# Kernel optimization log

Hardware: AMD Instinct MI355X
Metric: run time of the kernel (lower is better)

## Reference

```python
import jax, jax.numpy as jnp
import numpy as np

B, L, D, H = 4, 2048, 256, 8
FF = 128  # ff_intermediary_depth hard-coded in module
EPS = 1e-5


def layer_norm(x, g, b):
    mu = jnp.mean(x, axis=-1, keepdims=True)
    var = jnp.mean(jnp.square(x - mu), axis=-1, keepdims=True)
    return (x - mu) * jax.lax.rsqrt(var + EPS) * g + b


def setup_inputs() -> dict:
    key = jax.random.key(0)
    ks = jax.random.split(key, 8)
    s = 1.0 / np.sqrt(D)
    return {
        "seq": jax.random.normal(ks[0], (B, L, D), dtype=jnp.float32),
        "Wq": jax.random.normal(ks[1], (D, D * H), dtype=jnp.float32) * s,
        "Wk": jax.random.normal(ks[2], (D, D * H), dtype=jnp.float32) * s,
        "Wv": jax.random.normal(ks[3], (D, D * H), dtype=jnp.float32) * s,
        "Wo": jax.random.normal(ks[4], (D * H, D), dtype=jnp.float32) * (1.0 / np.sqrt(D * H)),
        "ln1_g": jnp.ones((D,), jnp.float32),
        "ln1_b": jnp.zeros((D,), jnp.float32),
        "W1": jax.random.normal(ks[5], (D, FF), dtype=jnp.float32) * s,
        "b1": jnp.zeros((FF,), jnp.float32),
        "W2": jax.random.normal(ks[6], (FF, D), dtype=jnp.float32) * (1.0 / np.sqrt(FF)),
        "b2": jnp.zeros((D,), jnp.float32),
        "ln2_g": jnp.ones((D,), jnp.float32),
        "ln2_b": jnp.zeros((D,), jnp.float32),
    }


def reference(seq, Wq, Wk, Wv, Wo, ln1_g, ln1_b, W1, b1, W2, b2, ln2_g, ln2_b):
    b, l, d = seq.shape
    # per-head dim equals full depth d (module quirk)
    q = (seq @ Wq).reshape(b, l, H, d)
    k = (seq @ Wk).reshape(b, l, H, d)
    v = (seq @ Wv).reshape(b, l, H, d)
    scores = jnp.einsum('bqhd,bkhd->bhqk', q, k) / jnp.sqrt(jnp.float32(d))
    a = jax.nn.softmax(scores, axis=-1)
    heads = jnp.einsum('bhqk,bkhd->bqhd', a, v).reshape(b, l, H * d)
    att_out = heads @ Wo
    x = layer_norm(seq + att_out, ln1_g, ln1_b)
    ff = jax.nn.relu(x @ W1 + b1) @ W2 + b2
    return layer_norm(x + ff, ln2_g, ln2_b)
```

## Files before the change

kernel.cpp:

```cpp
#include <hip/hip_runtime.h>


typedef unsigned short u16;
typedef unsigned int   u32;
typedef __bf16 bf16x8 __attribute__((ext_vector_type(8)));
typedef float  f32x4  __attribute__((ext_vector_type(4)));

#define MFMA(a, b, c) __builtin_amdgcn_mfma_f32_16x16x32_bf16(a, b, c, 0, 0, 0)

__device__ __forceinline__ float b2f(u16 h) {
  return __uint_as_float(((u32)h) << 16);
}
__device__ __forceinline__ u16 f2b(float f) {
  u32 u = __float_as_uint(f);
  u += 0x7FFFu + ((u >> 16) & 1u);
  return (u16)(u >> 16);
}
__device__ __forceinline__ bf16x8 ldb8(const u16* p) { return *(const bf16x8*)p; }

typedef const __attribute__((address_space(1))) u32* gas1_t;
typedef __attribute__((address_space(3))) u32* las3_t;
__device__ __forceinline__ void gload_lds16(const u16* g, u16* lds_base) {
  __builtin_amdgcn_global_load_lds((gas1_t)(const void*)g,
                                   (las3_t)(void*)lds_base, 16, 0, 0);
}

__device__ __forceinline__ int detect_f32(const void* seq) {
  const u32* s = (const u32*)seq;
  int cnt = 0;
  #pragma unroll
  for (int i = 0; i < 64; i++) {
    u32 e = (s[i] >> 7) & 0xFFu;
    cnt += (e >= 100u && e <= 140u) ? 1 : 0;
  }
  return cnt < 48;
}

__device__ __forceinline__ u16 ldw(const void* W, size_t idx, int isf32) {
  return isf32 ? f2b(((const float*)W)[idx]) : ((const u16*)W)[idx];
}

__global__ __launch_bounds__(256) void ingest_kernel(
    const void* __restrict__ seq, const void* __restrict__ g1,
    const void* __restrict__ be1, const void* __restrict__ b1,
    const void* __restrict__ b2v, const void* __restrict__ g2,
    const void* __restrict__ be2, u16* __restrict__ sbuf,
    u16* __restrict__ vecs) {
  int isf32 = detect_f32(seq);
  int bx = blockIdx.x, tid = threadIdx.x;
  if (bx < 2048) {
    size_t i = (size_t)bx * 1024 + tid * 4;
    if (isf32) {
      const float* sp = (const float*)seq;
      u16 o0 = f2b(sp[i]), o1 = f2b(sp[i + 1]), o2 = f2b(sp[i + 2]), o3 = f2b(sp[i + 3]);
      uint2 ov; ov.x = (u32)o0 | ((u32)o1 << 16); ov.y = (u32)o2 | ((u32)o3 << 16);
      *(uint2*)(sbuf + i) = ov;
    } else {
      *(uint2*)(sbuf + i) = ((const uint2*)seq)[i >> 2];
    }
  } else {
    int t = bx - 2048;
    const void* src; int n;
    switch (t) {
      case 0: src = g1;  n = 256; break;
      case 1: src = be1; n = 256; break;
      case 2: src = b1;  n = 128; break;
      case 3: src = b2v; n = 256; break;
      case 4: src = g2;  n = 256; break;
      default: src = be2; n = 256; break;
    }
    if (tid < n) vecs[t * 256 + tid] = ldw(src, tid, isf32);
  }
}

__global__ __launch_bounds__(256) void pack_kernel(
    const void* __restrict__ Wq, const void* __restrict__ Wk,
    const void* __restrict__ Wv, const void* __restrict__ Wo,
    const void* __restrict__ W1, const void* __restrict__ W2,
    const void* __restrict__ seq,
    u16* __restrict__ pWq, u16* __restrict__ pWk, u16* __restrict__ pWv,
    u16* __restrict__ pWo, u16* __restrict__ pW1, u16* __restrict__ pW2) {
  int isf32 = detect_f32(seq);
  const void* W; u16* P; int K, N;
  switch (blockIdx.y) {
    case 0: W = Wq; P = pWq; K = 256;  N = 2048; break;
    case 1: W = Wk; P = pWk; K = 256;  N = 2048; break;
    case 2: W = Wv; P = pWv; K = 256;  N = 2048; break;
    case 3: W = Wo; P = pWo; K = 2048; N = 256;  break;
    case 4: W = W1; P = pW1; K = 256;  N = 128;  break;
    default: W = W2; P = pW2; K = 128; N = 256;  break;
  }
  int t = blockIdx.x * 256 + threadIdx.x;
  int total = (K >> 5) * (N >> 4) * 64;
  if (t >= total) return;
  int lane = t & 63, f = t >> 6;
  int NT = N >> 4;
  int kt = f / NT, nt = f - kt * NT;
  int row0 = kt * 32 + ((lane >> 4) << 3);
  int col = nt * 16 + (lane & 15);
  u16 e[8];
  #pragma unroll
  for (int j = 0; j < 8; j++) e[j] = ldw(W, (size_t)(row0 + j) * N + col, isf32);
  uint4 u;
  u.x = (u32)e[0] | ((u32)e[1] << 16);
  u.y = (u32)e[2] | ((u32)e[3] << 16);
  u.z = (u32)e[4] | ((u32)e[5] << 16);
  u.w = (u32)e[6] | ((u32)e[7] << 16);
  *(uint4*)(P + ((size_t)f * 64 + lane) * 8) = u;
}

__global__ __launch_bounds__(256) void qkv_kernel(
    const u16* __restrict__ X,
    const u16* __restrict__ pWq, const u16* __restrict__ pWk,
    const u16* __restrict__ pWv,
    u16* __restrict__ Qo, u16* __restrict__ Ko, u16* __restrict__ Vo,
    int ntbase, int hc) {
  __shared__ u16 blds[64 * 512];
  const u16* Pw = (blockIdx.z == 0) ? pWq : ((blockIdx.z == 1) ? pWk : pWv);
  u16* Out = (blockIdx.z == 0) ? Qo : ((blockIdx.z == 1) ? Ko : Vo);
  int tid = threadIdx.x, lane = tid & 63, w = tid >> 6;
  int nt0 = ntbase + blockIdx.x * 8;
  #pragma unroll
  for (int i = 0; i < 16; i++) {
    int u = tid + i * 256;
    int fl = u >> 6, q = u & 63;
    int kt = fl >> 3, nt = fl & 7;
    ((uint4*)blds)[u] = ((const uint4*)Pw)[(size_t)(kt * 128 + nt0 + nt) * 64 + q];
  }
  __syncthreads();
  int m0 = blockIdx.y * 128 + w * 32;
  f32x4 acc[2][8] = {};
  #pragma unroll
  for (int kt = 0; kt < 8; kt++) {
    bf16x8 a0 = ldb8(X + (size_t)(m0 + (lane & 15)) * 256 + kt * 32 + (lane >> 4) * 8);
    bf16x8 a1 = ldb8(X + (size_t)(m0 + 16 + (lane & 15)) * 256 + kt * 32 + (lane >> 4) * 8);
    const u16* bp = blds + (size_t)kt * 8 * 512 + (size_t)lane * 8;
    #pragma unroll
    for (int nt = 0; nt < 8; nt++) {
      bf16x8 b = ldb8(bp + nt * 512);
      acc[0][nt] = MFMA(a0, b, acc[0][nt]);
      acc[1][nt] = MFMA(a1, b, acc[1][nt]);
    }
  }
  int isv = (blockIdx.z == 2);
  int hl = blockIdx.x >> 1;
  int dd0 = (blockIdx.x & 1) * 128;
  int m0b = blockIdx.y * 128;
  int bi = m0b >> 11, l0 = m0b & 2047;
  __syncthreads();
  if (!isv) {
    #pragma unroll
    for (int mt = 0; mt < 2; mt++)
      #pragma unroll
      for (int nt = 0; nt < 8; nt++)
        #pragma unroll
        for (int r = 0; r < 4; r++)
          blds[(w * 32 + mt * 16 + (lane >> 4) * 4 + r) * 136 + nt * 16 + (lane & 15)] =
              f2b(acc[mt][nt][r]);
    __syncthreads();
    #pragma unroll
    for (int i = 0; i < 8; i++) {
      int c = tid + i * 256;
      int mloc = c >> 4, q = c & 15;
      uint4 v = *(uint4*)(blds + mloc * 136 + q * 8);
      *(uint4*)(Out + ((size_t)(bi * hc + hl) * 2048 + l0 + mloc) * 256 + dd0 + q * 8) = v;
    }
  } else {
    #pragma unroll
    for (int mt = 0; mt < 2; mt++)
      #pragma unroll
      for (int nt = 0; nt < 8; nt++)
        #pragma unroll
        for (int r = 0; r < 4; r++)
          blds[(nt * 16 + (lane & 15)) * 136 + w * 32 + mt * 16 + (lane >> 4) * 4 + r] =
              f2b(acc[mt][nt][r]);
    __syncthreads();
    #pragma unroll
    for (int i = 0; i < 8; i++) {
      int c = tid + i * 256;
      int nloc = c >> 4, q = c & 15;
      uint4 v = *(uint4*)(blds + nloc * 136 + q * 8);
      *(uint4*)(Out + ((size_t)(bi * hc + hl) * 256 + dd0 + nloc) * 2048 + l0 + q * 8) = v;
    }
  }
}

__global__ __launch_bounds__(256, 2) void attn_kernel(
    const u16* __restrict__ Q, const u16* __restrict__ K,
    const u16* __restrict__ Vt, u16* __restrict__ O, int nbh) {
  __shared__ u16 kbuf[2 * 8192];
  __shared__ u16 vbuf[2 * 8192];
  __shared__ u16 plds[4 * 1280];
  int tid = threadIdx.x, lane = tid & 63, w = tid >> 6;
  int bi2 = blockIdx.x;
  int bh, qt;
  if (nbh >= 8) {
    int G = nbh >> 3;
    bh = (bi2 & 7) * G + (bi2 >> 3) % G;
    qt = bi2 / (8 * G);
  } else {
    bh = bi2 % nbh; qt = bi2 / nbh;
  }
  const u16* Qb  = Q  + (size_t)bh * 2048 * 256;
  const u16* Kb  = K  + (size_t)bh * 2048 * 256;
  const u16* Vtb = Vt + (size_t)bh * 256 * 2048;
  u16* Ob = O + (size_t)bh * 2048 * 256;
  int q0 = qt * 128 + w * 32;
  bf16x8 qf[2][8];
  #pragma unroll
  for (int qq = 0; qq < 2; qq++)
    #pragma unroll
    for (int kt = 0; kt < 8; kt++)
      qf[qq][kt] = ldb8(Qb + (size_t)(q0 + qq * 16 + (lane & 15)) * 256 +
                        kt * 32 + (lane >> 4) * 8);
  f32x4 o[2][16] = {};
  float lsum[2] = {0.f, 0.f};
  const float cexp = 0.0625f * 1.44269504088896f;
  u16* pl = plds + (size_t)w * 1280;

  #pragma unroll
  for (int j = 0; j < 4; j++) {
    int f = w * 4 + j;
    gload_lds16(Kb + (size_t)((f >> 3) * 16 + (lane & 15)) * 256 +
                    (f & 7) * 32 + (lane >> 4) * 8,
                kbuf + f * 512);
    gload_lds16(Vtb + (size_t)(f * 16 + (lane & 15)) * 2048 + (lane >> 4) * 8,
                vbuf + f * 512);
  }

  for (int t = 0; t < 64; t++) {
    int s0 = t * 32;
    asm volatile("s_waitcnt vmcnt(0)\ns_barrier" ::: "memory");
    if (t < 63) {
      int nb = (t + 1) & 1;
      #pragma unroll
      for (int j = 0; j < 4; j++) {
        int f = w * 4 + j;
        gload_lds16(Kb + (size_t)(s0 + 32 + (f >> 3) * 16 + (lane & 15)) * 256 +
                        (f & 7) * 32 + (lane >> 4) * 8,
                    kbuf + nb * 8192 + f * 512);
        gload_lds16(Vtb + (size_t)(f * 16 + (lane & 15)) * 2048 + s0 + 32 +
                        (lane >> 4) * 8,
                    vbuf + nb * 8192 + f * 512);
      }
    }
    const u16* kb = kbuf + (t & 1) * 8192;
    f32x4 s[2][2] = {};
    __builtin_amdgcn_s_setprio(1);
    #pragma unroll
    for (int ntk = 0; ntk < 2; ntk++)
      #pragma unroll
      for (int kt = 0; kt < 8; kt++) {
        bf16x8 a = ldb8(kb + (size_t)(ntk * 8 + kt) * 512 + lane * 8);
        s[0][ntk] = MFMA(a, qf[0][kt], s[0][ntk]);
        s[1][ntk] = MFMA(a, qf[1][kt], s[1][ntk]);
      }
    __builtin_amdgcn_s_setprio(0);
    #pragma unroll
    for (int qq = 0; qq < 2; qq++)
      #pragma unroll
      for (int ntk = 0; ntk < 2; ntk++) {
        float p0 = exp2f(s[qq][ntk][0] * cexp);
        float p1 = exp2f(s[qq][ntk][1] * cexp);
        float p2 = exp2f(s[qq][ntk][2] * cexp);
        float p3 = exp2f(s[qq][ntk][3] * cexp);
        lsum[qq] += (p0 + p1) + (p2 + p3);
        uint2 pk;
        pk.x = (u32)f2b(p0) | ((u32)f2b(p1) << 16);
        pk.y = (u32)f2b(p2) | ((u32)f2b(p3) << 16);
        *(uint2*)(pl + (qq * 16 + (lane & 15)) * 40 + 16 * ntk + 4 * (lane >> 4)) = pk;
      }
    asm volatile("s_waitcnt lgkmcnt(0)" ::: "memory");
    bf16x8 pa0 = ldb8(pl + (lane & 15) * 40 + (lane >> 4) * 8);
    bf16x8 pa1 = ldb8(pl + (16 + (lane & 15)) * 40 + (lane >> 4) * 8);
    const u16* vb0 = vbuf + (t & 1) * 8192;
    __builtin_amdgcn_s_setprio(1);
    #pragma unroll
    for (int nt = 0; nt < 16; nt++) {
      bf16x8 vb = ldb8(vb0 + (size_t)nt * 512 + lane * 8);
      o[0][nt] = MFMA(vb, pa0, o[0][nt]);
      o[1][nt] = MFMA(vb, pa1, o[1][nt]);
    }
    __builtin_amdgcn_s_setprio(0);
  }
  u16* el = kbuf + w * 1152;
  __syncthreads();
  #pragma unroll
  for (int qq = 0; qq < 2; qq++) {
    float l = lsum[qq];
    l += __shfl_xor(l, 16);
    l += __shfl_xor(l, 32);
    float linv = 1.0f / l;
    #pragma unroll
    for (int g = 0; g < 4; g++) {
      if (qq || g) asm volatile("s_waitcnt lgkmcnt(0)" ::: "memory");
      #pragma unroll
      for (int t2 = 0; t2 < 4; t2++) {
        int nt = g * 4 + t2;
        uint2 pk;
        pk.x = (u32)f2b(o[qq][nt][0] * linv) | ((u32)f2b(o[qq][nt][1] * linv) << 16);
        pk.y = (u32)f2b(o[qq][nt][2] * linv) | ((u32)f2b(o[qq][nt][3] * linv) << 16);
        *(uint2*)(el + (lane & 15) * 72 + t2 * 16 + 4 * (lane >> 4)) = pk;
      }
      asm volatile("s_waitcnt lgkmcnt(0)" ::: "memory");
      #pragma unroll
      for (int rep = 0; rep < 2; rep++) {
        int ch = lane + rep * 64;
        int row = ch >> 3, c8 = ch & 7;
        uint4 v = *(uint4*)(el + row * 72 + c8 * 8);
        *(uint4*)(Ob + (size_t)(q0 + qq * 16 + row) * 256 + g * 64 + c8 * 8) = v;
      }
    }
  }
}

__global__ __launch_bounds__(256) void accum_ln1_kernel(
    const u16* __restrict__ Oc, const u16* __restrict__ pWo,
    const u16* __restrict__ sbuf, const u16* __restrict__ vecs,
    u16* __restrict__ xout) {
  __shared__ u16 blds[64 * 512];
  int tid = threadIdx.x, lane = tid & 63, w = tid >> 6;
  int m0 = blockIdx.x * 64 + w * 16;
  int arow = m0 + (lane & 15);
  int bq = arow >> 11, lrow = arow & 2047;
  f32x4 acc[16] = {};
  for (int k0 = 0; k0 < 64; k0 += 4) {
    __syncthreads();
    #pragma unroll
    for (int i = 0; i < 16; i++) {
      int u = tid + i * 256;
      int fl = u >> 6, q = u & 63;
      int ktg = k0 + (fl >> 4), nt = fl & 15;
      ((uint4*)blds)[u] = ((const uint4*)pWo)[(size_t)(ktg * 16 + nt) * 64 + q];
    }
    __syncthreads();
    #pragma unroll
    for (int kl = 0; kl < 4; kl++) {
      int ktl = k0 + kl;
      int hl = ktl >> 3;
      int d0 = (ktl & 7) * 32 + (lane >> 4) * 8;
      bf16x8 a = ldb8(Oc + ((size_t)(bq * 8 + hl) * 2048 + lrow) * 256 + d0);
      const u16* bp = blds + (size_t)kl * 16 * 512 + (size_t)lane * 8;
      #pragma unroll
      for (int nt = 0; nt < 16; nt++) {
        bf16x8 b = ldb8(bp + nt * 512);
        acc[nt] = MFMA(a, b, acc[nt]);
      }
    }
  }
  int rbase = m0 + (lane >> 4) * 4;
  #pragma unroll
  for (int nt = 0; nt < 16; nt++) {
    int d = nt * 16 + (lane & 15);
    #pragma unroll
    for (int r = 0; r < 4; r++)
      acc[nt][r] += b2f(sbuf[(size_t)(rbase + r) * 256 + d]);
  }
  float mu[4], rs[4];
  #pragma unroll
  for (int r = 0; r < 4; r++) {
    float sm = 0.f;
    #pragma unroll
    for (int nt = 0; nt < 16; nt++) sm += acc[nt][r];
    sm += __shfl_xor(sm, 1); sm += __shfl_xor(sm, 2);
    sm += __shfl_xor(sm, 4); sm += __shfl_xor(sm, 8);
    mu[r] = sm * (1.0f / 256.0f);
    float v = 0.f;
    #pragma unroll
    for (int nt = 0; nt < 16; nt++) { float dd = acc[nt][r] - mu[r]; v += dd * dd; }
    v += __shfl_xor(v, 1); v += __shfl_xor(v, 2);
    v += __shfl_xor(v, 4); v += __shfl_xor(v, 8);
    rs[r] = rsqrtf(v * (1.0f / 256.0f) + 1e-5f);
  }
  #pragma unroll
  for (int nt = 0; nt < 16; nt++) {
    int d = nt * 16 + (lane & 15);
    float gg = b2f(vecs[d]), bb = b2f(vecs[256 + d]);
    #pragma unroll
    for (int r = 0; r < 4; r++)
      xout[(size_t)(rbase + r) * 256 + d] = f2b((acc[nt][r] - mu[r]) * rs[r] * gg + bb);
  }
}

__global__ __launch_bounds__(256) void accum_kernel(
    const u16* __restrict__ Oc, const u16* __restrict__ pWo,
    float* __restrict__ att_out, int kt0, int hc) {
  __shared__ u16 blds[64 * 512];
  int tid = threadIdx.x, lane = tid & 63, w = tid >> 6;
  int m0 = blockIdx.x * 64 + w * 16;
  int arow = m0 + (lane & 15);
  int bq = arow >> 11, lrow = arow & 2047;
  int ktn = hc * 8;
  f32x4 acc[16] = {};
  for (int k0 = 0; k0 < ktn; k0 += 4) {
    __syncthreads();
    #pragma unroll
    for (int i = 0; i < 16; i++) {
      int u = tid + i * 256;
      int fl = u >> 6, q = u & 63;
      int ktg = kt0 + k0 + (fl >> 4), nt = fl & 15;
      ((uint4*)blds)[u] = ((const uint4*)pWo)[(size_t)(ktg * 16 + nt) * 64 + q];
    }
    __syncthreads();
    #pragma unroll
    for (int kl = 0; kl < 4; kl++) {
      int ktl = k0 + kl;
      int hl = ktl >> 3;
      int d0 = (ktl & 7) * 32 + (lane >> 4) * 8;
      bf16x8 a = ldb8(Oc + ((size_t)(bq * hc + hl) * 2048 + lrow) * 256 + d0);
      const u16* bp = blds + (size_t)kl * 16 * 512 + (size_t)lane * 8;
      #pragma unroll
      for (int nt = 0; nt < 16; nt++) {
        bf16x8 b = ldb8(bp + nt * 512);
        acc[nt] = MFMA(a, b, acc[nt]);
      }
    }
  }
  int rbase = m0 + (lane >> 4) * 4;
  #pragma unroll
  for (int nt = 0; nt < 16; nt++) {
    int d = nt * 16 + (lane & 15);
    #pragma unroll
    for (int r = 0; r < 4; r++)
      att_out[(size_t)(rbase + r) * 256 + d] += acc[nt][r];
  }
}

__global__ __launch_bounds__(256) void ln1_kernel(
    const float* __restrict__ att_out, const u16* __restrict__ sbuf,
    const u16* __restrict__ vecs, u16* __restrict__ xout) {
  int tid = threadIdx.x, lane = tid & 63, w = tid >> 6;
  int row = blockIdx.x * 4 + w;
  const float* ar = att_out + (size_t)row * 256;
  f32x4 a = *(const f32x4*)(ar + lane * 4);
  uint2 sv = *(const uint2*)(sbuf + (size_t)row * 256 + lane * 4);
  float y[4];
  y[0] = a[0] + b2f((u16)(sv.x & 0xFFFF));
  y[1] = a[1] + b2f((u16)(sv.x >> 16));
  y[2] = a[2] + b2f((u16)(sv.y & 0xFFFF));
  y[3] = a[3] + b2f((u16)(sv.y >> 16));
  float sm = y[0] + y[1] + y[2] + y[3];
  sm += __shfl_xor(sm, 1);  sm += __shfl_xor(sm, 2);  sm += __shfl_xor(sm, 4);
  sm += __shfl_xor(sm, 8);  sm += __shfl_xor(sm, 16); sm += __shfl_xor(sm, 32);
  float mu = sm * (1.0f / 256.0f);
  float v = 0.f;
  #pragma unroll
  for (int j = 0; j < 4; j++) { float d = y[j] - mu; v += d * d; }
  v += __shfl_xor(v, 1);  v += __shfl_xor(v, 2);  v += __shfl_xor(v, 4);
  v += __shfl_xor(v, 8);  v += __shfl_xor(v, 16); v += __shfl_xor(v, 32);
  float rs = rsqrtf(v * (1.0f / 256.0f) + 1e-5f);
  u16 o[4];
  #pragma unroll
  for (int j = 0; j < 4; j++) {
    int d = lane * 4 + j;
    o[j] = f2b((y[j] - mu) * rs * b2f(vecs[d]) + b2f(vecs[256 + d]));
  }
  uint2 ov; ov.x = (u32)o[0] | ((u32)o[1] << 16); ov.y = (u32)o[2] | ((u32)o[3] << 16);
  *(uint2*)(xout + (size_t)row * 256 + lane * 4) = ov;
}

__global__ __launch_bounds__(256) void ffn_ln2_kernel(
    const u16* __restrict__ x, const u16* __restrict__ pW1,
    const u16* __restrict__ pW2, const u16* __restrict__ vecs,
    const void* __restrict__ seq, void* __restrict__ out) {
  __shared__ u16 hbuf[4 * 16 * 136];
  int isf32 = detect_f32(seq);
  int tid = threadIdx.x, lane = tid & 63, w = tid >> 6;
  int m0 = blockIdx.x * 64 + w * 16;
  int arow = m0 + (lane & 15);
  u16* hb = hbuf + w * 16 * 136;
  f32x4 acc1[8] = {};
  #pragma unroll
  for (int kt = 0; kt < 8; kt++) {
    bf16x8 a = ldb8(x + (size_t)arow * 256 + kt * 32 + (lane >> 4) * 8);
    const u16* bp = pW1 + ((size_t)kt * 8 * 64 + lane) * 8;
    #pragma unroll
    for (int nt = 0; nt < 8; nt++) {
      bf16x8 b = ldb8(bp + nt * 512);
      acc1[nt] = MFMA(a, b, acc1[nt]);
    }
  }
  #pragma unroll
  for (int nt = 0; nt < 8; nt++) {
    int col = nt * 16 + (lane & 15);
    float bb = b2f(vecs[512 + col]);
    #pragma unroll
    for (int r = 0; r < 4; r++) {
      float h = fmaxf(acc1[nt][r] + bb, 0.f);
      hb[((lane >> 4) * 4 + r) * 136 + col] = f2b(h);
    }
  }
  __syncthreads();
  f32x4 acc2[16] = {};
  #pragma unroll
  for (int ks = 0; ks < 4; ks++) {
    bf16x8 a = ldb8(hb + (lane & 15) * 136 + ks * 32 + (lane >> 4) * 8);
    const u16* bp = pW2 + ((size_t)ks * 16 * 64 + lane) * 8;
    #pragma unroll
    for (int nt = 0; nt < 16; nt++) {
      bf16x8 b = ldb8(bp + nt * 512);
      acc2[nt] = MFMA(a, b, acc2[nt]);
    }
  }
  int rbase = m0 + (lane >> 4) * 4;
  #pragma unroll
  for (int nt = 0; nt < 16; nt++) {
    int d = nt * 16 + (lane & 15);
    float bb = b2f(vecs[768 + d]);
    #pragma unroll
    for (int r = 0; r < 4; r++)
      acc2[nt][r] += bb + b2f(x[(size_t)(rbase + r) * 256 + d]);
  }
  float mu[4], rs[4];
  #pragma unroll
  for (int r = 0; r < 4; r++) {
    float sm = 0.f;
    #pragma unroll
    for (int nt = 0; nt < 16; nt++) sm += acc2[nt][r];
    sm += __shfl_xor(sm, 1); sm += __shfl_xor(sm, 2);
    sm += __shfl_xor(sm, 4); sm += __shfl_xor(sm, 8);
    mu[r] = sm * (1.0f / 256.0f);
    float v = 0.f;
    #pragma unroll
    for (int nt = 0; nt < 16; nt++) { float dd = acc2[nt][r] - mu[r]; v += dd * dd; }
    v += __shfl_xor(v, 1); v += __shfl_xor(v, 2);
    v += __shfl_xor(v, 4); v += __shfl_xor(v, 8);
    rs[r] = rsqrtf(v * (1.0f / 256.0f) + 1e-5f);
  }
  #pragma unroll
  for (int nt = 0; nt < 16; nt++) {
    int d = nt * 16 + (lane & 15);
    float gg = b2f(vecs[1024 + d]), bb = b2f(vecs[1280 + d]);
    #pragma unroll
    for (int r = 0; r < 4; r++) {
      float val = (acc2[nt][r] - mu[r]) * rs[r] * gg + bb;
      size_t idx = (size_t)(rbase + r) * 256 + d;
      if (isf32) ((float*)out)[idx] = val;
      else       ((u16*)out)[idx]   = f2b(val);
    }
  }
}

__global__ __launch_bounds__(256) void sentinel_kernel(void* out, int n,
                                                       const void* seq) {
  int isf32 = detect_f32(seq);
  int i = blockIdx.x * 256 + threadIdx.x;
  if (i < n) {
    if (isf32) ((float*)out)[i] = 777.0f;
    else       ((u16*)out)[i]   = 0x4442;
  }
}

extern "C" void kernel_launch(void* const* d_in, const int* in_sizes, int n_in,
                              void* d_out, int out_size, void* d_ws, size_t ws_size,
                              hipStream_t stream) {
  (void)in_sizes; (void)n_in;
  const void* seq  = d_in[0];
  const void* Wq   = d_in[1];
  const void* Wk   = d_in[2];
  const void* Wv   = d_in[3];
  const void* Wo   = d_in[4];
  const void* g1   = d_in[5];
  const void* be1  = d_in[6];
  const void* W1   = d_in[7];
  const void* b1   = d_in[8];
  const void* W2   = d_in[9];
  const void* b2   = d_in[10];
  const void* g2   = d_in[11];
  const void* be2  = d_in[12];

  size_t o = 0;
  u16* ws = (u16*)d_ws;
  u16* pWq = ws + o; o += 524288;
  u16* pWk = ws + o; o += 524288;
  u16* pWv = ws + o; o += 524288;
  u16* pWo = ws + o; o += 524288;
  u16* pW1 = ws + o; o += 32768;
  u16* pW2 = ws + o; o += 32768;
  float* att = (float*)(ws + o); o += 4194304;
  u16* xb   = ws + o; o += 2097152;
  u16* sbuf = ws + o; o += 2097152;
  u16* vecs = ws + o; o += 2048;
  size_t fixed_elems = o;

  int hc = 0;
  for (int c = 8; c >= 1; c >>= 1) {
    size_t need = (fixed_elems + (size_t)4 * c * 2097152) * 2;
    if (need <= ws_size) { hc = c; break; }
  }
  if (hc == 0) {
    sentinel_kernel<<<dim3((out_size + 255) / 256), 256, 0, stream>>>(
        d_out, out_size, seq);
    return;
  }
  u16* Qc = ws + o; o += (size_t)hc * 2097152;
  u16* Kc = ws + o; o += (size_t)hc * 2097152;
  u16* Vc = ws + o; o += (size_t)hc * 2097152;
  u16* Oc = ws + o;

  ingest_kernel<<<dim3(2054), 256, 0, stream>>>(seq, g1, be1, b1, b2, g2, be2,
                                                sbuf, vecs);
  pack_kernel<<<dim3(256, 6), 256, 0, stream>>>(Wq, Wk, Wv, Wo, W1, W2, seq,
                                                pWq, pWk, pWv, pWo, pW1, pW2);
  if (hc == 8) {
    qkv_kernel<<<dim3(16, 64, 3), 256, 0, stream>>>(
        sbuf, pWq, pWk, pWv, Qc, Kc, Vc, 0, 8);
    attn_kernel<<<dim3(32 * 16), 256, 0, stream>>>(Qc, Kc, Vc, Oc, 32);
    accum_ln1_kernel<<<dim3(128), 256, 0, stream>>>(Oc, pWo, sbuf, vecs, xb);
  } else {
    hipMemsetAsync(att, 0, 2097152 * sizeof(float), stream);
    int nchunks = 8 / hc;
    for (int c = 0; c < nchunks; c++) {
      int nbh = 4 * hc;
      qkv_kernel<<<dim3(2 * hc, 64, 3), 256, 0, stream>>>(
          sbuf, pWq, pWk, pWv, Qc, Kc, Vc, c * hc * 16, hc);
      attn_kernel<<<dim3(nbh * 16), 256, 0, stream>>>(Qc, Kc, Vc, Oc, nbh);
      accum_kernel<<<dim3(128), 256, 0, stream>>>(Oc, pWo, att, c * hc * 8, hc);
    }
    ln1_kernel<<<dim3(2048), 256, 0, stream>>>(att, sbuf, vecs, xb);
  }
  ffn_ln2_kernel<<<dim3(128), 256, 0, stream>>>(xb, pW1, pW2, vecs, seq,
                                                (void*)d_out);
}
```

Before: 372.7 us.

## Software-pipeline attention loop so PV MFMAs of previous tile overlap QK

Restructures the flash-attention inner loop so that the P·V product for tile t-1 is issued right after the QK^T MFMAs of tile t. The exp/softmax work of tile t can then overlap with matrix-core work instead of serializing. V loads are shifted one iteration later to match, and an epilogue handles the final tile. The P buffer is reused across the iteration boundary, which relies on the barrier for ordering and raises register pressure.

```diff
diff --git a/kernel.cpp b/kernel.cpp
--- a/kernel.cpp
+++ b/kernel.cpp
@@ -224,25 +224,26 @@
     gload_lds16(Kb + (size_t)((f >> 3) * 16 + (lane & 15)) * 256 +
                     (f & 7) * 32 + (lane >> 4) * 8,
                 kbuf + f * 512);
-    gload_lds16(Vtb + (size_t)(f * 16 + (lane & 15)) * 2048 + (lane >> 4) * 8,
-                vbuf + f * 512);
   }
 
   for (int t = 0; t < 64; t++) {
     int s0 = t * 32;
     asm volatile("s_waitcnt vmcnt(0)\ns_barrier" ::: "memory");
-    if (t < 63) {
-      int nb = (t + 1) & 1;
-      #pragma unroll
-      for (int j = 0; j < 4; j++) {
-        int f = w * 4 + j;
+    #pragma unroll
+    for (int j = 0; j < 4; j++) {
+      int f = w * 4 + j;
+      if (t < 63)
         gload_lds16(Kb + (size_t)(s0 + 32 + (f >> 3) * 16 + (lane & 15)) * 256 +
                         (f & 7) * 32 + (lane >> 4) * 8,
-                    kbuf + nb * 8192 + f * 512);
-        gload_lds16(Vtb + (size_t)(f * 16 + (lane & 15)) * 2048 + s0 + 32 +
-                        (lane >> 4) * 8,
-                    vbuf + nb * 8192 + f * 512);
-      }
+                    kbuf + ((t + 1) & 1) * 8192 + f * 512);
+      gload_lds16(Vtb + (size_t)(f * 16 + (lane & 15)) * 2048 + s0 +
+                      (lane >> 4) * 8,
+                  vbuf + (t & 1) * 8192 + f * 512);
+    }
+    bf16x8 pa0, pa1;
+    if (t) {
+      pa0 = ldb8(pl + (lane & 15) * 40 + (lane >> 4) * 8);
+      pa1 = ldb8(pl + (16 + (lane & 15)) * 40 + (lane >> 4) * 8);
     }
     const u16* kb = kbuf + (t & 1) * 8192;
     f32x4 s[2][2] = {};
@@ -255,6 +256,15 @@
         s[0][ntk] = MFMA(a, qf[0][kt], s[0][ntk]);
         s[1][ntk] = MFMA(a, qf[1][kt], s[1][ntk]);
       }
+    if (t) {
+      const u16* vb0 = vbuf + ((t - 1) & 1) * 8192;
+      #pragma unroll
+      for (int nt = 0; nt < 16; nt++) {
+        bf16x8 vb = ldb8(vb0 + (size_t)nt * 512 + lane * 8);
+        o[0][nt] = MFMA(vb, pa0, o[0][nt]);
+        o[1][nt] = MFMA(vb, pa1, o[1][nt]);
+      }
+    }
     __builtin_amdgcn_s_setprio(0);
     #pragma unroll
     for (int qq = 0; qq < 2; qq++)
@@ -270,10 +280,12 @@
         pk.y = (u32)f2b(p2) | ((u32)f2b(p3) << 16);
         *(uint2*)(pl + (qq * 16 + (lane & 15)) * 40 + 16 * ntk + 4 * (lane >> 4)) = pk;
       }
-    asm volatile("s_waitcnt lgkmcnt(0)" ::: "memory");
+  }
+  asm volatile("s_waitcnt vmcnt(0)\ns_barrier" ::: "memory");
+  {
     bf16x8 pa0 = ldb8(pl + (lane & 15) * 40 + (lane >> 4) * 8);
     bf16x8 pa1 = ldb8(pl + (16 + (lane & 15)) * 40 + (lane >> 4) * 8);
-    const u16* vb0 = vbuf + (t & 1) * 8192;
+    const u16* vb0 = vbuf + 8192;
     __builtin_amdgcn_s_setprio(1);
     #pragma unroll
     for (int nt = 0; nt < 16; nt++) {
```

New measurement: 389.3 us. +4.5%, slower.
